# Kernel tuning notes

Hardware: AMD Instinct MI355X
Metric: run time of the kernel (lower is better)

The kernel has to match this reference:

```python
import jax, jax.numpy as jnp
import numpy as np
from jax import lax

PRE_NMS_TOPN = 6000
POST_NMS_TOPN = 1500
NMS_IOU_THRESHOLD = 0.7
VARIANCES = (0.1, 0.1, 0.2, 0.2)
TOTAL_ANCHORS = 200000
BATCH = 8


def setup_inputs() -> dict:
    key = jax.random.key(0)
    k1, k2, k3, k4 = jax.random.split(key, 4)
    rpn_bbox_deltas = jax.random.normal(k1, (BATCH, TOTAL_ANCHORS, 4), dtype=jnp.float32)
    rpn_probs = jax.random.uniform(k2, (BATCH, TOTAL_ANCHORS), dtype=jnp.float32)
    # anchors: valid normalized [y1, x1, y2, x2] boxes
    ctr = jax.random.uniform(k3, (TOTAL_ANCHORS, 2), dtype=jnp.float32)          # (cy, cx)
    hw = jax.random.uniform(k4, (TOTAL_ANCHORS, 2), dtype=jnp.float32,
                            minval=0.02, maxval=0.3)                              # (h, w)
    anchors = jnp.concatenate([ctr - 0.5 * hw, ctr + 0.5 * hw], axis=-1)
    return {"rpn_bbox_deltas": rpn_bbox_deltas, "rpn_probs": rpn_probs, "anchors": anchors}


def _nms_single(boxes):
    # boxes: [P, 4] sorted by descending score; greedy NMS, return [POST, 4] zero-padded,
    # coordinates clipped to [0, 1] (tf combined_non_max_suppression clip_boxes=True default).
    P = boxes.shape[0]
    y1, x1, y2, x2 = boxes[:, 0], boxes[:, 1], boxes[:, 2], boxes[:, 3]
    area = (y2 - y1) * (x2 - x1)
    iy1 = jnp.maximum(y1[:, None], y1[None, :])
    ix1 = jnp.maximum(x1[:, None], x1[None, :])
    iy2 = jnp.minimum(y2[:, None], y2[None, :])
    ix2 = jnp.minimum(x2[:, None], x2[None, :])
    inter = jnp.maximum(iy2 - iy1, 0.0) * jnp.maximum(ix2 - ix1, 0.0)
    iou = inter / (area[:, None] + area[None, :] - inter)  # [P, P]
    idx = jnp.arange(P)

    def body(i, keep):
        suppressed = keep[i] & (iou[i] > NMS_IOU_THRESHOLD) & (idx > i)
        return keep & ~suppressed

    keep = lax.fori_loop(0, P, body, jnp.ones((P,), dtype=bool))

    rank = jnp.cumsum(keep) - 1                      # position among kept boxes
    valid = keep & (rank < POST_NMS_TOPN)
    tgt = jnp.where(valid, rank, POST_NMS_TOPN)      # overflow slot for dropped boxes
    clipped = jnp.clip(boxes, 0.0, 1.0)
    out = jnp.zeros((POST_NMS_TOPN + 1, 4), dtype=boxes.dtype)
    out = out.at[tgt].set(jnp.where(valid[:, None], clipped, 0.0))
    return out[:POST_NMS_TOPN]


def reference(rpn_bbox_deltas, rpn_probs, anchors):
    variances = jnp.asarray(VARIANCES, dtype=rpn_bbox_deltas.dtype)
    deltas = rpn_bbox_deltas * variances                       # [B, A, 4]

    anc_w = anchors[:, 3] - anchors[:, 1]
    anc_h = anchors[:, 2] - anchors[:, 0]
    anc_cx = anchors[:, 1] + 0.5 * anc_w
    anc_cy = anchors[:, 0] + 0.5 * anc_h

    bw = jnp.exp(deltas[..., 3]) * anc_w
    bh = jnp.exp(deltas[..., 2]) * anc_h
    bcx = deltas[..., 1] * anc_w + anc_cx
    bcy = deltas[..., 0] * anc_h + anc_cy

    y1 = bcy - 0.5 * bh
    x1 = bcx - 0.5 * bw
    y2 = bh + y1
    x2 = bw + x1
    rpn_bboxes = jnp.stack([y1, x1, y2, x2], axis=-1)          # [B, A, 4]

    _, pre_indices = lax.top_k(rpn_probs, PRE_NMS_TOPN)        # [B, P], sorted desc
    pre_boxes = jnp.take_along_axis(rpn_bboxes, pre_indices[..., None], axis=1)  # [B, P, 4]

    roi_bboxes = jax.vmap(_nms_single)(pre_boxes)              # [B, POST, 4]
    return roi_bboxes
```

## Files before the change

### kernel.cpp

```cpp
#include <hip/hip_runtime.h>
#include <hip/hip_bf16.h>


#define TOTAL   200000
#define NBATCH  8
#define PRE     6000
#define POST    1500
#define NW      94
#define CAP     8192
#define NQ      (TOTAL/4)
#define GR      256
#define NGFAST  9
#define PLANES  960
#define HB      32

__device__ __forceinline__ unsigned int prob_key(float p) {
    return __float_as_uint(__fadd_rn(p, 1.0f)) & 0x7FFFFFu;
}

__global__ __launch_bounds__(1024) void k_hist256(const float* __restrict__ probs,
                                                  unsigned int* __restrict__ histS,
                                                  unsigned int* __restrict__ gcount) {
    const int b = blockIdx.y;
    const int bx = blockIdx.x;
    const int tid = threadIdx.x;
    __shared__ unsigned int h[256];
    if (tid < 256) h[tid] = 0u;
    if (bx == 0 && tid < 256) gcount[b * 256 + tid] = 0u;
    __syncthreads();
    const float4* p4 = (const float4*)(probs + (size_t)b * TOTAL);
    for (int i4 = bx * 1024 + tid; i4 < NQ; i4 += HB * 1024) {
        float4 v = p4[i4];
        atomicAdd(&h[prob_key(v.x) >> 15], 1u);
        atomicAdd(&h[prob_key(v.y) >> 15], 1u);
        atomicAdd(&h[prob_key(v.z) >> 15], 1u);
        atomicAdd(&h[prob_key(v.w) >> 15], 1u);
    }
    __syncthreads();
    if (tid < 256) histS[((size_t)b * HB + bx) * 256 + tid] = h[tid];
}

__global__ __launch_bounds__(1024) void k_collect(const float* __restrict__ probs,
                                                  const unsigned int* __restrict__ histS,
                                                  unsigned long long* __restrict__ keys,
                                                  unsigned int* __restrict__ gcount) {
    const int b = blockIdx.y;
    const int tid = threadIdx.x;
    __shared__ unsigned int S[257];
    __shared__ unsigned int lcnt[256];
    __shared__ unsigned int gbase[256];
    __shared__ unsigned int s_B;
    if (tid == 0) { s_B = 0u; S[256] = 0u; }
    if (tid < 256) {
        unsigned int s = 0u;
        const unsigned int* hb = histS + (size_t)b * HB * 256 + tid;
#pragma unroll
        for (int k = 0; k < HB; ++k) s += hb[k * 256];
        S[tid] = s; lcnt[tid] = 0u;
    }
    __syncthreads();
    for (int off = 1; off < 256; off <<= 1) {
        unsigned int v = 0u;
        if (tid < 256 && tid + off < 256) v = S[tid + off];
        __syncthreads();
        if (tid < 256) S[tid] += v;
        __syncthreads();
    }
    if (tid < 256 && S[tid] >= PRE) atomicMax(&s_B, (unsigned int)tid);
    __syncthreads();
    const unsigned int B = s_B;
    unsigned int kk[4], ii[4], tt[4], lp[4]; int n = 0;
    const int i4 = blockIdx.x * 1024 + tid;
    if (i4 < NQ) {
        float4 v = ((const float4*)(probs + (size_t)b * TOTAL))[i4];
        float pv[4] = {v.x, v.y, v.z, v.w};
#pragma unroll
        for (int j = 0; j < 4; ++j) {
            unsigned int key = prob_key(pv[j]);
            unsigned int t = key >> 15;
            if (t >= B) {
                kk[n] = key; ii[n] = (unsigned int)(i4 * 4 + j); tt[n] = t;
                lp[n] = atomicAdd(&lcnt[t], 1u);
                ++n;
            }
        }
    }
    __syncthreads();
    if (tid < 256 && lcnt[tid] > 0u)
        gbase[tid] = atomicAdd(&gcount[b * 256 + tid], lcnt[tid]);
    __syncthreads();
    for (int j = 0; j < n; ++j) {
        unsigned int t = tt[j];
        unsigned int pos = S[t + 1] + gbase[t] + lp[j];
        if (pos < CAP)
            keys[(size_t)b * CAP + pos] =
                ((unsigned long long)kk[j] << 32) | (unsigned long long)(~ii[j]);
    }
}

__global__ __launch_bounds__(256) void k_rank(const unsigned long long* __restrict__ keys,
                                              const unsigned int* __restrict__ histS,
                                              const float* __restrict__ deltas,
                                              const float* __restrict__ anchors,
                                              float4* __restrict__ boxes) {
    const int b   = blockIdx.y;
    const int rel = blockIdx.x;
    const int tid = threadIdx.x;
    __shared__ unsigned int S[257];
    __shared__ unsigned int s_B;
    __shared__ unsigned long long K2[CAP];
    __shared__ unsigned int CNT[512];
    __shared__ unsigned int W[512];
    __shared__ unsigned int P[256];
    if (tid == 0) { s_B = 0u; S[256] = 0u; }
    {
        unsigned int s = 0u;
        const unsigned int* hb = histS + (size_t)b * HB * 256 + tid;
#pragma unroll
        for (int k = 0; k < HB; ++k) s += hb[k * 256];
        S[tid] = s;
    }
    __syncthreads();
    for (int off = 1; off < 256; off <<= 1) {
        unsigned int v = (tid + off < 256) ? S[tid + off] : 0u;
        __syncthreads();
        S[tid] += v;
        __syncthreads();
    }
    if (S[tid] >= PRE) atomicMax(&s_B, (unsigned int)tid);
    __syncthreads();
    const int B = (int)s_B;
    const int t = B + rel;
    if (t > 255) return;
    const unsigned int lo = (rel == 15) ? 0u : S[t + 1];
    unsigned int hi = S[t]; if (hi > CAP) hi = CAP;
    if (hi <= lo) return;
    const unsigned int n = hi - lo;
    CNT[tid] = 0u; CNT[tid + 256] = 0u;
    __syncthreads();
    const unsigned long long* kb = keys + (size_t)b * CAP + lo;
    for (unsigned int i = tid; i < n; i += 256u) {
        const unsigned int key23 = (unsigned int)(kb[i] >> 32);
        const unsigned int bin = (rel == 15) ? (key23 >> 14) : ((key23 >> 6) & 511u);
        atomicAdd(&CNT[bin], 1u);
    }
    __syncthreads();
    {
        const unsigned int c0 = CNT[2 * tid], c1 = CNT[2 * tid + 1];
        P[tid] = c0 + c1;
        __syncthreads();
        for (int off = 1; off < 256; off <<= 1) {
            unsigned int v = (tid + off < 256) ? P[tid + off] : 0u;
            __syncthreads();
            P[tid] += v;
            __syncthreads();
        }
        const unsigned int above = P[tid] - (c0 + c1);
        W[2 * tid + 1] = above;
        W[2 * tid]     = above + c1;
    }
    __syncthreads();
    for (unsigned int i = tid; i < n; i += 256u) {
        const unsigned long long k = kb[i];
        const unsigned int key23 = (unsigned int)(k >> 32);
        const unsigned int bin = (rel == 15) ? (key23 >> 14) : ((key23 >> 6) & 511u);
        const unsigned int slot = atomicAdd(&W[bin], 1u);
        K2[slot] = k;
    }
    __syncthreads();
    for (int s = tid; s < 512; s += 256) {
        const unsigned int st = (s < 511) ? W[s + 1] : 0u;
        const unsigned int en = W[s];
        for (unsigned int x = st; x + 1 < en; ++x) {
            unsigned long long best = K2[x]; unsigned int bi = x;
            for (unsigned int y = x + 1; y < en; ++y) {
                unsigned long long v = K2[y];
                if (v > best) { best = v; bi = y; }
            }
            if (bi != x) { K2[bi] = K2[x]; K2[x] = best; }
        }
    }
    __syncthreads();
    for (unsigned int r = tid; r < n; r += 256u) {
        const unsigned int grank = lo + r;
        if (grank >= PRE) continue;
        const unsigned long long k = K2[r];
        const unsigned int idx = ~(unsigned int)(k & 0xFFFFFFFFull);
        const float* d = deltas + ((size_t)b * TOTAL + (size_t)idx) * 4;
        const float* a = anchors + (size_t)idx * 4;
        float d0 = __fmul_rn(d[0], 0.1f), d1 = __fmul_rn(d[1], 0.1f);
        float d2 = __fmul_rn(d[2], 0.2f), d3 = __fmul_rn(d[3], 0.2f);
        float a0 = a[0], a1 = a[1], a2 = a[2], a3 = a[3];
        float aw = __fsub_rn(a3, a1), ah = __fsub_rn(a2, a0);
        float acx = __fadd_rn(a1, __fmul_rn(0.5f, aw));
        float acy = __fadd_rn(a0, __fmul_rn(0.5f, ah));
        float bw = __fmul_rn(expf(d3), aw);
        float bh = __fmul_rn(expf(d2), ah);
        float bcx = __fadd_rn(__fmul_rn(d1, aw), acx);
        float bcy = __fadd_rn(__fmul_rn(d0, ah), acy);
        float y1 = __fsub_rn(bcy, __fmul_rn(0.5f, bh));
        float x1 = __fsub_rn(bcx, __fmul_rn(0.5f, bw));
        float y2 = __fadd_rn(bh, y1);
        float x2 = __fadd_rn(bw, x1);
        boxes[(size_t)b * PRE + grank] = make_float4(y1, x1, y2, x2);
    }
}

__global__ __launch_bounds__(256) void k_mask(const float4* __restrict__ boxes,
                                              unsigned long long* __restrict__ maskT) {
    const int b  = blockIdx.z;
    const int by = blockIdx.y;
    const int bx = blockIdx.x;
    if (bx < by) return;
    const int tid = threadIdx.x;
    __shared__ float4 cbox[256];
    __shared__ float  cth[256];
    __shared__ float  cca[256];
    {
        int col = bx * 256 + tid;
        float4 cb = (col < PRE) ? boxes[(size_t)b * PRE + col] : make_float4(0.f, 0.f, 0.f, 0.f);
        cbox[tid] = cb;
        float ca = __fmul_rn(__fsub_rn(cb.z, cb.x), __fsub_rn(cb.w, cb.y));
        cca[tid] = ca;
        cth[tid] = __fmul_rn(0.4115f, ca);
    }
    __syncthreads();
    const int il = tid & 63;
    const int ws = tid >> 6;
    const int w  = bx * 4 + ws;
    if (w >= NW) return;
    const int ibase = by * 256 + il;
    float4 rb0, rb1, rb2, rb3;
    {
        const float4 z = make_float4(0.f, 0.f, 0.f, 0.f);
        rb0 = boxes[(size_t)b * PRE + ibase];
        rb1 = (ibase +  64 < PRE) ? boxes[(size_t)b * PRE + ibase +  64] : z;
        rb2 = (ibase + 128 < PRE) ? boxes[(size_t)b * PRE + ibase + 128] : z;
        rb3 = (ibase + 192 < PRE) ? boxes[(size_t)b * PRE + ibase + 192] : z;
    }
    const float ra0 = __fmul_rn(__fsub_rn(rb0.z, rb0.x), __fsub_rn(rb0.w, rb0.y));
    const float ra1 = __fmul_rn(__fsub_rn(rb1.z, rb1.x), __fsub_rn(rb1.w, rb1.y));
    const float ra2 = __fmul_rn(__fsub_rn(rb2.z, rb2.x), __fsub_rn(rb2.w, rb2.y));
    const float ra3 = __fmul_rn(__fsub_rn(rb3.z, rb3.x), __fsub_rn(rb3.w, rb3.y));
    const float rc0 = __fmul_rn(0.4115f, ra0);
    const float rc1 = __fmul_rn(0.4115f, ra1);
    const float rc2 = __fmul_rn(0.4115f, ra2);
    const float rc3 = __fmul_rn(0.4115f, ra3);
    unsigned long long bits0 = 0ull, bits1 = 0ull, bits2 = 0ull, bits3 = 0ull;
    const double M = 0x1.666667p-1;
#pragma unroll 8
    for (int jj = 0; jj < 64; ++jj) {
        const float4 cb = cbox[ws * 64 + jj];
        const float  th = cth[ws * 64 + jj];
#define ROWTEST(rb, ra, rc, bits)                                              \
        {                                                                      \
            float dy = __fsub_rn(fminf(rb.z, cb.z), fmaxf(rb.x, cb.x));        \
            float dx = __fsub_rn(fminf(rb.w, cb.w), fmaxf(rb.y, cb.y));        \
            float hh = fmaxf(dy, 0.0f);                                        \
            float in = __fmul_rn(hh, dx);                                      \
            if (in > __fadd_rn(rc, th)) {                                      \
                float ww2 = fmaxf(dx, 0.0f);                                   \
                float ix  = __fmul_rn(hh, ww2);                                \
                float un  = __fsub_rn(__fadd_rn(ra, cca[ws * 64 + jj]), ix);   \
                if ((double)ix >= M * (double)un) bits |= (1ull << jj);        \
            }                                                                  \
        }
        ROWTEST(rb0, ra0, rc0, bits0)
        ROWTEST(rb1, ra1, rc1, bits1)
        ROWTEST(rb2, ra2, rc2, bits2)
        ROWTEST(rb3, ra3, rc3, bits3)
#undef ROWTEST
    }
    const int jbase = w * 64;
#define ROWSTORE(k, bits)                                                      \
    {                                                                          \
        const int i = ibase + 64 * (k);                                        \
        if (i < PRE && w >= (i >> 6)) {                                        \
            unsigned long long bb = bits;                                      \
            if (jbase <= i) {                                                  \
                int nclear = i - jbase + 1;                                    \
                bb = (nclear >= 64) ? 0ull : (bb & (~0ull << nclear));         \
            }                                                                  \
            maskT[((size_t)b * NW + w) * PRE + i] = bb;                        \
        }                                                                      \
    }
    ROWSTORE(0, bits0)
    ROWSTORE(1, bits1)
    ROWSTORE(2, bits2)
    ROWSTORE(3, bits3)
#undef ROWSTORE
}

__device__ __forceinline__ unsigned long long rfl64(unsigned long long v) {
    unsigned int lo = (unsigned int)__builtin_amdgcn_readfirstlane((unsigned int)v);
    unsigned int hi = (unsigned int)__builtin_amdgcn_readfirstlane((unsigned int)(v >> 32));
    return ((unsigned long long)hi << 32) | (unsigned long long)lo;
}

__device__ __forceinline__ unsigned long long wor64(unsigned long long v) {
    int lo = (int)(unsigned int)v;
    int hi = (int)(unsigned int)(v >> 32);
    lo |= __builtin_amdgcn_ds_swizzle(lo, 0x041F); hi |= __builtin_amdgcn_ds_swizzle(hi, 0x041F);
    lo |= __builtin_amdgcn_ds_swizzle(lo, 0x081F); hi |= __builtin_amdgcn_ds_swizzle(hi, 0x081F);
    lo |= __builtin_amdgcn_ds_swizzle(lo, 0x101F); hi |= __builtin_amdgcn_ds_swizzle(hi, 0x101F);
    lo |= __builtin_amdgcn_ds_swizzle(lo, 0x201F); hi |= __builtin_amdgcn_ds_swizzle(hi, 0x201F);
    lo |= __builtin_amdgcn_ds_swizzle(lo, 0x401F); hi |= __builtin_amdgcn_ds_swizzle(hi, 0x401F);
    const unsigned int l = (unsigned int)__builtin_amdgcn_readlane(lo, 0)
                         | (unsigned int)__builtin_amdgcn_readlane(lo, 32);
    const unsigned int h = (unsigned int)__builtin_amdgcn_readlane(hi, 0)
                         | (unsigned int)__builtin_amdgcn_readlane(hi, 32);
    return ((unsigned long long)h << 32) | (unsigned long long)l;
}

#define DIDX(qr,qw) ((qr)*4 + (qw) - ((qr)*((qr)+1))/2)

__global__ __launch_bounds__(1024) void k_scan(const float4* __restrict__ boxes,
                                               const unsigned long long* __restrict__ maskT,
                                               float4* __restrict__ out) {
    const int b = blockIdx.x;
    const int tid = threadIdx.x;
    const int wv = tid >> 6;
    const int lane = tid & 63;
    __shared__ unsigned long long remw[2][4];
    __shared__ unsigned long long keptbm[96];
    __shared__ float4 boxbuf[2][GR];
    __shared__ float4 keptbox[POST];
    __shared__ unsigned int s_rank;
    __shared__ int s_done;
    __shared__ int s_sup;
    if (tid < 8) ((unsigned long long*)remw)[tid] = 0ull;
    if (tid < 96) keptbm[tid] = 0ull;
    if (tid == 0) { s_rank = 0u; s_done = 0; }
    const unsigned long long* mb = maskT + (size_t)b * NW * PRE;

    unsigned long long dCur[10];
    unsigned long long pend0 = 0ull, pend1 = 0ull;
    unsigned int rank = 0u;

    if (wv == 0) {
#pragma unroll
        for (int qr = 0; qr < 4; ++qr) {
            const int row = 64 * qr + lane;
#pragma unroll
            for (int qw = qr; qw < 4; ++qw)
                dCur[DIDX(qr, qw)] = mb[(size_t)qw * PRE + row];
        }
    } else if (wv == 1) {
#pragma unroll
        for (int q = 0; q < 4; ++q)
            boxbuf[0][64 * q + lane] = boxes[(size_t)b * PRE + 64 * q + lane];
    }
    __syncthreads();

    for (int g = 0; g < NGFAST; ++g) {
        const int r0 = g * GR;
        const int w0 = g * 4;
        if (wv > 0) {
            const int L = tid - 64;
            unsigned int* R = (unsigned int*)&remw[g & 1][0];
            if (pend0) {
                const int q = L >> 8;
                const int row = (g - 1) * GR + (L & 255);
                if ((keptbm[row >> 6] >> (row & 63)) & 1ull) {
                    atomicOr(&R[2 * q],     (unsigned int)pend0);
                    atomicOr(&R[2 * q + 1], (unsigned int)(pend0 >> 32));
                }
            }
            if (pend1) {
                const int row = (g - 1) * GR + 192 + L;
                if ((keptbm[row >> 6] >> (row & 63)) & 1ull) {
                    atomicOr(&R[6], (unsigned int)pend1);
                    atomicOr(&R[7], (unsigned int)(pend1 >> 32));
                }
            }
        }
        __syncthreads();

        if (wv == 0) {
            unsigned long long dNxt[10];
#pragma unroll
            for (int i = 0; i < 10; ++i) dNxt[i] = 0ull;
            if (g + 1 < NGFAST) {
                const int r0n = (g + 1) * GR, w0n = (g + 1) * 4;
#pragma unroll
                for (int qr = 0; qr < 4; ++qr) {
                    const int row = r0n + 64 * qr + lane;
                    const bool rok = row < PRE;
#pragma unroll
                    for (int qw = qr; qw < 4; ++qw) {
                        const int w = w0n + qw;
                        if (rok && w < NW)
                            dNxt[DIDX(qr, qw)] = mb[(size_t)w * PRE + row];
                    }
                }
            }
            unsigned long long av[4];
#pragma unroll
            for (int q = 0; q < 4; ++q) av[q] = remw[g & 1][q];
            if (lane < 4) remw[g & 1][lane] = 0ull;
#pragma unroll
            for (int q = 0; q < 4; ++q) {
                const int rq = r0 + 64 * q;
                const unsigned long long valid =
                    (rq >= PRE) ? 0ull
                    : ((rq + 64 <= PRE) ? ~0ull : ((~0ull) >> (64 - (PRE - rq))));
                av[q] = rfl64(~av[q]) & valid;
            }
            unsigned long long keptq[4];
            unsigned int base = rank;
#pragma unroll
            for (int q = 0; q < 4; ++q) {
                const unsigned long long avq = av[q];
                const unsigned long long W = dCur[DIDX(q, q)];
                unsigned long long kept = 0ull;
                if (avq != 0ull) {
                    unsigned long long m = ((avq >> lane) & 1ull) ? W : 0ull;
                    const unsigned long long U = wor64(m);
                    const unsigned long long C = avq & ~U;
                    kept = C;
                    unsigned long long rem = avq & U;
                    if (rem != 0ull) {
                        unsigned long long mc = ((C >> lane) & 1ull) ? W : 0ull;
                        const unsigned long long UC = wor64(mc);
                        unsigned long long av2 = rem & ~UC;
                        const unsigned int wlo = (unsigned int)W;
                        const unsigned int whi = (unsigned int)(W >> 32);
                        while (av2) {
                            const int i2 = __ffsll((long long)av2) - 1;
                            const unsigned long long bit = 1ull << i2;
                            kept |= bit;
                            const unsigned long long Wi =
                                ((unsigned long long)(unsigned int)__builtin_amdgcn_readlane(whi, i2) << 32)
                                | (unsigned long long)(unsigned int)__builtin_amdgcn_readlane(wlo, i2);
                            av2 &= ~(Wi | bit);
                        }
                    }
                }
                keptq[q] = kept;
                if (q < 3 && kept != 0ull) {
                    const bool on = ((kept >> lane) & 1ull) != 0ull;
                    unsigned long long c1 = 0ull, c2 = 0ull, c3 = 0ull;
                    if (q == 0 && on) { c1 = dCur[DIDX(0,1)]; c2 = dCur[DIDX(0,2)]; c3 = dCur[DIDX(0,3)]; }
                    if (q == 1 && on) { c2 = dCur[DIDX(1,2)]; c3 = dCur[DIDX(1,3)]; }
                    if (q == 2 && on) { c3 = dCur[DIDX(2,3)]; }
                    if (q == 0) av[1] &= ~wor64(c1);
                    if (q <= 1) av[2] &= ~wor64(c2);
                    av[3] &= ~wor64(c3);
                }
                if ((kept >> lane) & 1ull) {
                    const unsigned int r =
                        base + (unsigned int)__popcll(kept & ((1ull << lane) - 1ull));
                    if (r < POST) {
                        const float4 v = boxbuf[g & 1][64 * q + lane];
                        keptbox[r] = v;
                        float4 cl;
                        cl.x = fminf(fmaxf(v.x, 0.f), 1.f);
                        cl.y = fminf(fmaxf(v.y, 0.f), 1.f);
                        cl.z = fminf(fmaxf(v.z, 0.f), 1.f);
                        cl.w = fminf(fmaxf(v.w, 0.f), 1.f);
                        out[(size_t)b * POST + r] = cl;
                    }
                }
                base += (unsigned int)__popcll(kept);
            }
            if (lane == 0) {
                keptbm[w0 + 0] = keptq[0];
                keptbm[w0 + 1] = keptq[1];
                keptbm[w0 + 2] = keptq[2];
                keptbm[w0 + 3] = keptq[3];
                s_rank = base;
                s_done = (base >= POST) ? 1 : 0;
            }
            rank = base;
#pragma unroll
            for (int i = 0; i < 10; ++i) dCur[i] = dNxt[i];
        } else {
            const int L = tid - 64;
            pend0 = 0ull; pend1 = 0ull;
            if (g + 1 < NGFAST) {
                const int w0n = (g + 1) * 4;
                if (wv == 1) {
#pragma unroll
                    for (int q = 0; q < 4; ++q) {
                        const int row = (g + 1) * GR + 64 * q + lane;
                        boxbuf[(g + 1) & 1][64 * q + lane] =
                            (row < PRE) ? boxes[(size_t)b * PRE + row]
                                        : make_float4(0.f, 0.f, 0.f, 0.f);
                    }
                }
                const bool ok1 = (w0n + 1 < NW), ok2 = (w0n + 2 < NW), ok3 = (w0n + 3 < NW);
                unsigned long long a0 = 0ull, a1 = 0ull, a2 = 0ull, a3 = 0ull;
                const int rlim = g * GR;
                for (int row = L; row < rlim; row += PLANES) {
                    const unsigned long long km =
                        ((keptbm[row >> 6] >> (row & 63)) & 1ull) ? ~0ull : 0ull;
                    const unsigned long long* cb = mb + row;
                    const unsigned long long v0 = cb[(size_t)(w0n + 0) * PRE];
                    const unsigned long long v1 = ok1 ? cb[(size_t)(w0n + 1) * PRE] : 0ull;
                    const unsigned long long v2 = ok2 ? cb[(size_t)(w0n + 2) * PRE] : 0ull;
                    const unsigned long long v3 = ok3 ? cb[(size_t)(w0n + 3) * PRE] : 0ull;
                    a0 |= v0 & km; a1 |= v1 & km; a2 |= v2 & km; a3 |= v3 & km;
                }
                {
                    unsigned int* R = (unsigned int*)&remw[(g + 1) & 1][0];
                    if (a0) { atomicOr(&R[0], (unsigned int)a0); atomicOr(&R[1], (unsigned int)(a0 >> 32)); }
                    if (a1) { atomicOr(&R[2], (unsigned int)a1); atomicOr(&R[3], (unsigned int)(a1 >> 32)); }
                    if (a2) { atomicOr(&R[4], (unsigned int)a2); atomicOr(&R[5], (unsigned int)(a2 >> 32)); }
                    if (a3) { atomicOr(&R[6], (unsigned int)a3); atomicOr(&R[7], (unsigned int)(a3 >> 32)); }
                }
                {
                    const int q = L >> 8;
                    const int w = w0n + q;
                    if (w < NW)
                        pend0 = mb[(size_t)w * PRE + (size_t)(g * GR + (L & 255))];
                }
                if (L < 64) {
                    const int w = w0n + 3;
                    if (w < NW)
                        pend1 = mb[(size_t)w * PRE + (size_t)(g * GR + 192 + L)];
                }
            }
        }
        __syncthreads();
        if (s_done) break;
    }

    if (!s_done) {
        unsigned int rk = s_rank;
        const double M = 0x1.666667p-1;
        for (int row = NGFAST * GR; row < PRE && rk < POST; ++row) {
            if (tid == 0) s_sup = 0;
            __syncthreads();
            const float4 rb = boxes[(size_t)b * PRE + row];
            const float ra = __fmul_rn(__fsub_rn(rb.z, rb.x), __fsub_rn(rb.w, rb.y));
            int sup = 0;
            for (unsigned int j = (unsigned int)tid; j < rk; j += 1024u) {
                const float4 kb = keptbox[j];
                float dy = __fsub_rn(fminf(rb.z, kb.z), fmaxf(rb.x, kb.x));
                float dx = __fsub_rn(fminf(rb.w, kb.w), fmaxf(rb.y, kb.y));
                float hh = fmaxf(dy, 0.f);
                float ww = fmaxf(dx, 0.f);
                float ix = __fmul_rn(hh, ww);
                float ka = __fmul_rn(__fsub_rn(kb.z, kb.x), __fsub_rn(kb.w, kb.y));
                float un = __fsub_rn(__fadd_rn(ka, ra), ix);
                if ((double)ix >= M * (double)un) { sup = 1; break; }
            }
            if (sup) atomicOr(&s_sup, 1);
            __syncthreads();
            if (!s_sup) {
                if (tid == 0) {
                    keptbox[rk] = rb;
                    float4 cl;
                    cl.x = fminf(fmaxf(rb.x, 0.f), 1.f);
                    cl.y = fminf(fmaxf(rb.y, 0.f), 1.f);
                    cl.z = fminf(fmaxf(rb.z, 0.f), 1.f);
                    cl.w = fminf(fmaxf(rb.w, 0.f), 1.f);
                    out[(size_t)b * POST + rk] = cl;
                }
                ++rk;
                __syncthreads();
            }
        }
        if (tid == 0) s_rank = rk;
        __syncthreads();
    }

    unsigned int filled = s_rank; if (filled > POST) filled = POST;
    for (unsigned int r = filled + (unsigned int)tid; r < POST; r += 1024u)
        out[(size_t)b * POST + r] = make_float4(0.f, 0.f, 0.f, 0.f);
}

extern "C" void kernel_launch(void* const* d_in, const int* in_sizes, int n_in,
                              void* d_out, int out_size, void* d_ws, size_t ws_size,
                              hipStream_t stream) {
    const float* deltas  = (const float*)d_in[0];
    const float* probs   = (const float*)d_in[1];
    const float* anchors = (const float*)d_in[2];
    char* ws = (char*)d_ws;
    unsigned int*       histS  = (unsigned int*)(ws);
    unsigned int*       gcount = (unsigned int*)(ws + 262144);
    unsigned long long* keys   = (unsigned long long*)(ws + 270336);
    float4*             boxes  = (float4*)(ws + 270336 + 524288);
    unsigned long long* maskT  = (unsigned long long*)(ws + 270336 + 524288 + 768000);
    float4* out = (float4*)d_out;

    k_hist256<<<dim3(HB, NBATCH), 1024, 0, stream>>>(probs, histS, gcount);
    k_collect<<<dim3((NQ + 1023) / 1024, NBATCH), 1024, 0, stream>>>(probs, histS, keys, gcount);
    k_rank<<<dim3(16, NBATCH), 256, 0, stream>>>(keys, histS, deltas, anchors, boxes);
    k_mask<<<dim3(NGFAST, NGFAST, NBATCH), 256, 0, stream>>>(boxes, maskT);
    k_scan<<<NBATCH, 1024, 0, stream>>>(boxes, maskT, out);
}
```

Before: 144.0 us.

## Fuse histogram and candidate collection into one pass with speculative top-bin buckets

```diff
diff --git a/kernel.cpp b/kernel.cpp
--- a/kernel.cpp
+++ b/kernel.cpp
@@ -13,93 +13,49 @@
 #define NGFAST  9
 #define PLANES  960
 #define HB      32
+#define KB0     246
+#define SUBCAP  160
 
 __device__ __forceinline__ unsigned int prob_key(float p) {
     return __float_as_uint(__fadd_rn(p, 1.0f)) & 0x7FFFFFu;
 }
 
-__global__ __launch_bounds__(1024) void k_hist256(const float* __restrict__ probs,
+__global__ __launch_bounds__(1024) void k_histsel(const float* __restrict__ probs,
                                                   unsigned int* __restrict__ histS,
-                                                  unsigned int* __restrict__ gcount) {
+                                                  unsigned long long* __restrict__ abuf) {
     const int b = blockIdx.y;
     const int bx = blockIdx.x;
     const int tid = threadIdx.x;
     __shared__ unsigned int h[256];
+    __shared__ unsigned int lcnt[10];
     if (tid < 256) h[tid] = 0u;
-    if (bx == 0 && tid < 256) gcount[b * 256 + tid] = 0u;
+    if (tid < 10) lcnt[tid] = 0u;
     __syncthreads();
     const float4* p4 = (const float4*)(probs + (size_t)b * TOTAL);
     for (int i4 = bx * 1024 + tid; i4 < NQ; i4 += HB * 1024) {
         float4 v = p4[i4];
-        atomicAdd(&h[prob_key(v.x) >> 15], 1u);
-        atomicAdd(&h[prob_key(v.y) >> 15], 1u);
-        atomicAdd(&h[prob_key(v.z) >> 15], 1u);
-        atomicAdd(&h[prob_key(v.w) >> 15], 1u);
+        float pv[4] = {v.x, v.y, v.z, v.w};
+#pragma unroll
+        for (int j = 0; j < 4; ++j) {
+            const unsigned int key = prob_key(pv[j]);
+            const unsigned int t = key >> 15;
+            atomicAdd(&h[t], 1u);
+            if (t >= KB0) {
+                const unsigned int slot = atomicAdd(&lcnt[t - KB0], 1u);
+                if (slot < SUBCAP)
+                    abuf[(((size_t)b * 10 + (t - KB0)) * HB + bx) * SUBCAP + slot] =
+                        ((unsigned long long)key << 32)
+                        | (unsigned long long)(~(unsigned int)(i4 * 4 + j));
+            }
+        }
     }
     __syncthreads();
     if (tid < 256) histS[((size_t)b * HB + bx) * 256 + tid] = h[tid];
 }
 
-__global__ __launch_bounds__(1024) void k_collect(const float* __restrict__ probs,
-                                                  const unsigned int* __restrict__ histS,
-                                                  unsigned long long* __restrict__ keys,
-                                                  unsigned int* __restrict__ gcount) {
-    const int b = blockIdx.y;
-    const int tid = threadIdx.x;
-    __shared__ unsigned int S[257];
-    __shared__ unsigned int lcnt[256];
-    __shared__ unsigned int gbase[256];
-    __shared__ unsigned int s_B;
-    if (tid == 0) { s_B = 0u; S[256] = 0u; }
-    if (tid < 256) {
-        unsigned int s = 0u;
-        const unsigned int* hb = histS + (size_t)b * HB * 256 + tid;
-#pragma unroll
-        for (int k = 0; k < HB; ++k) s += hb[k * 256];
-        S[tid] = s; lcnt[tid] = 0u;
-    }
-    __syncthreads();
-    for (int off = 1; off < 256; off <<= 1) {
-        unsigned int v = 0u;
-        if (tid < 256 && tid + off < 256) v = S[tid + off];
-        __syncthreads();
-        if (tid < 256) S[tid] += v;
-        __syncthreads();
-    }
-    if (tid < 256 && S[tid] >= PRE) atomicMax(&s_B, (unsigned int)tid);
-    __syncthreads();
-    const unsigned int B = s_B;
-    unsigned int kk[4], ii[4], tt[4], lp[4]; int n = 0;
-    const int i4 = blockIdx.x * 1024 + tid;
-    if (i4 < NQ) {
-        float4 v = ((const float4*)(probs + (size_t)b * TOTAL))[i4];
-        float pv[4] = {v.x, v.y, v.z, v.w};
-#pragma unroll
-        for (int j = 0; j < 4; ++j) {
-            unsigned int key = prob_key(pv[j]);
-            unsigned int t = key >> 15;
-            if (t >= B) {
-                kk[n] = key; ii[n] = (unsigned int)(i4 * 4 + j); tt[n] = t;
-                lp[n] = atomicAdd(&lcnt[t], 1u);
-                ++n;
-            }
-        }
-    }
-    __syncthreads();
-    if (tid < 256 && lcnt[tid] > 0u)
-        gbase[tid] = atomicAdd(&gcount[b * 256 + tid], lcnt[tid]);
-    __syncthreads();
-    for (int j = 0; j < n; ++j) {
-        unsigned int t = tt[j];
-        unsigned int pos = S[t + 1] + gbase[t] + lp[j];
-        if (pos < CAP)
-            keys[(size_t)b * CAP + pos] =
-                ((unsigned long long)kk[j] << 32) | (unsigned long long)(~ii[j]);
-    }
-}
-
-__global__ __launch_bounds__(256) void k_rank(const unsigned long long* __restrict__ keys,
+__global__ __launch_bounds__(256) void k_rank(const unsigned long long* __restrict__ abuf,
                                               const unsigned int* __restrict__ histS,
+                                              const float* __restrict__ probs,
                                               const float* __restrict__ deltas,
                                               const float* __restrict__ anchors,
                                               float4* __restrict__ boxes) {
@@ -108,11 +64,13 @@
     const int tid = threadIdx.x;
     __shared__ unsigned int S[257];
     __shared__ unsigned int s_B;
-    __shared__ unsigned long long K2[CAP];
+    __shared__ int s_slow;
     __shared__ unsigned int CNT[512];
     __shared__ unsigned int W[512];
     __shared__ unsigned int P[256];
-    if (tid == 0) { s_B = 0u; S[256] = 0u; }
+    __shared__ unsigned int SZ[HB];
+    __shared__ unsigned long long K2[CAP];
+    if (tid == 0) { s_B = 0u; S[256] = 0u; s_slow = 0; }
     {
         unsigned int s = 0u;
         const unsigned int* hb = histS + (size_t)b * HB * 256 + tid;
@@ -130,19 +88,88 @@
     if (S[tid] >= PRE) atomicMax(&s_B, (unsigned int)tid);
     __syncthreads();
     const int B = (int)s_B;
+    if (tid == 0 && B < KB0) s_slow = 1;
+    for (int x = tid; x < (256 - KB0) * HB; x += 256) {
+        const int t = KB0 + x / HB, blk = x % HB;
+        if (t >= B && histS[((size_t)b * HB + blk) * 256 + t] > SUBCAP) atomicOr(&s_slow, 1);
+    }
+    if (tid >= KB0 && tid >= B && (S[tid] - S[tid + 1]) > 2048u) atomicOr(&s_slow, 1);
+    __syncthreads();
+
+    if (s_slow) {
+        if (rel != 0) return;
+        W[tid] = S[tid + 1];
+        for (int x = tid; x < CAP; x += 256) K2[x] = 0ull;
+        __syncthreads();
+        const float4* p4 = (const float4*)(probs + (size_t)b * TOTAL);
+        for (int i4 = tid; i4 < NQ; i4 += 256) {
+            float4 v = p4[i4];
+            float pv[4] = {v.x, v.y, v.z, v.w};
+#pragma unroll
+            for (int j = 0; j < 4; ++j) {
+                const unsigned int key = prob_key(pv[j]);
+                const unsigned int tt = key >> 15;
+                if ((int)tt >= B) {
+                    const unsigned int pos = atomicAdd(&W[tt], 1u);
+                    if (pos < CAP)
+                        K2[pos] = ((unsigned long long)key << 32)
+                                  | (unsigned long long)(~(unsigned int)(i4 * 4 + j));
+                }
+            }
+        }
+        __syncthreads();
+        for (int k = 2; k <= CAP; k <<= 1) {
+            for (int j = k >> 1; j > 0; j >>= 1) {
+                for (int x = tid; x < CAP; x += 256) {
+                    const int ixj = x ^ j;
+                    if (ixj > x) {
+                        const bool asc = ((x & k) != 0);
+                        const unsigned long long a = K2[x], c = K2[ixj];
+                        if (asc ? (a > c) : (a < c)) { K2[x] = c; K2[ixj] = a; }
+                    }
+                }
+                __syncthreads();
+            }
+        }
+        for (unsigned int r = tid; r < PRE; r += 256u) {
+            const unsigned long long k = K2[r];
+            const unsigned int idx = ~(unsigned int)(k & 0xFFFFFFFFull);
+            const float* d = deltas + ((size_t)b * TOTAL + (size_t)idx) * 4;
+            const float* a = anchors + (size_t)idx * 4;
+            float d0 = __fmul_rn(d[0], 0.1f), d1 = __fmul_rn(d[1], 0.1f);
+            float d2 = __fmul_rn(d[2], 0.2f), d3 = __fmul_rn(d[3], 0.2f);
+            float a0 = a[0], a1 = a[1], a2 = a[2], a3 = a[3];
+            float aw = __fsub_rn(a3, a1), ah = __fsub_rn(a2, a0);
+            float acx = __fadd_rn(a1, __fmul_rn(0.5f, aw));
+            float acy = __fadd_rn(a0, __fmul_rn(0.5f, ah));
+            float bw = __fmul_rn(expf(d3), aw);
+            float bh = __fmul_rn(expf(d2), ah);
+            float bcx = __fadd_rn(__fmul_rn(d1, aw), acx);
+            float bcy = __fadd_rn(__fmul_rn(d0, ah), acy);
+            float y1 = __fsub_rn(bcy, __fmul_rn(0.5f, bh));
+            float x1 = __fsub_rn(bcx, __fmul_rn(0.5f, bw));
+            float y2 = __fadd_rn(bh, y1);
+            float x2 = __fadd_rn(bw, x1);
+            boxes[(size_t)b * PRE + r] = make_float4(y1, x1, y2, x2);
+        }
+        return;
+    }
+
     const int t = B + rel;
     if (t > 255) return;
-    const unsigned int lo = (rel == 15) ? 0u : S[t + 1];
-    unsigned int hi = S[t]; if (hi > CAP) hi = CAP;
-    if (hi <= lo) return;
-    const unsigned int n = hi - lo;
+    const unsigned int n = S[t] - S[t + 1];
+    if (n == 0u) return;
+    const unsigned int lo = S[t + 1];
+    if (tid < HB) SZ[tid] = histS[((size_t)b * HB + tid) * 256 + t];
     CNT[tid] = 0u; CNT[tid + 256] = 0u;
     __syncthreads();
-    const unsigned long long* kb = keys + (size_t)b * CAP + lo;
-    for (unsigned int i = tid; i < n; i += 256u) {
-        const unsigned int key23 = (unsigned int)(kb[i] >> 32);
-        const unsigned int bin = (rel == 15) ? (key23 >> 14) : ((key23 >> 6) & 511u);
-        atomicAdd(&CNT[bin], 1u);
+    const unsigned long long* tb = abuf + ((size_t)b * 10 + (t - KB0)) * HB * SUBCAP;
+    for (int x = tid; x < HB * SUBCAP; x += 256) {
+        const int blk = x / SUBCAP, off = x % SUBCAP;
+        if ((unsigned int)off < SZ[blk]) {
+            const unsigned int key23 = (unsigned int)(tb[x] >> 32);
+            atomicAdd(&CNT[(key23 >> 6) & 511u], 1u);
+        }
     }
     __syncthreads();
     {
@@ -160,12 +187,14 @@
         W[2 * tid]     = above + c1;
     }
     __syncthreads();
-    for (unsigned int i = tid; i < n; i += 256u) {
-        const unsigned long long k = kb[i];
-        const unsigned int key23 = (unsigned int)(k >> 32);
-        const unsigned int bin = (rel == 15) ? (key23 >> 14) : ((key23 >> 6) & 511u);
-        const unsigned int slot = atomicAdd(&W[bin], 1u);
-        K2[slot] = k;
+    for (int x = tid; x < HB * SUBCAP; x += 256) {
+        const int blk = x / SUBCAP, off = x % SUBCAP;
+        if ((unsigned int)off < SZ[blk]) {
+            const unsigned long long k = tb[x];
+            const unsigned int key23 = (unsigned int)(k >> 32);
+            const unsigned int slot = atomicAdd(&W[(key23 >> 6) & 511u], 1u);
+            K2[slot] = k;
+        }
     }
     __syncthreads();
     for (int s = tid; s < 512; s += 256) {
@@ -577,16 +606,14 @@
     const float* probs   = (const float*)d_in[1];
     const float* anchors = (const float*)d_in[2];
     char* ws = (char*)d_ws;
-    unsigned int*       histS  = (unsigned int*)(ws);
-    unsigned int*       gcount = (unsigned int*)(ws + 262144);
-    unsigned long long* keys   = (unsigned long long*)(ws + 270336);
-    float4*             boxes  = (float4*)(ws + 270336 + 524288);
-    unsigned long long* maskT  = (unsigned long long*)(ws + 270336 + 524288 + 768000);
+    unsigned int*       histS = (unsigned int*)(ws);
+    unsigned long long* abuf  = (unsigned long long*)(ws + 262144);
+    float4*             boxes = (float4*)(ws + 3538944);
+    unsigned long long* maskT = (unsigned long long*)(ws + 4306944);
     float4* out = (float4*)d_out;
 
-    k_hist256<<<dim3(HB, NBATCH), 1024, 0, stream>>>(probs, histS, gcount);
-    k_collect<<<dim3((NQ + 1023) / 1024, NBATCH), 1024, 0, stream>>>(probs, histS, keys, gcount);
-    k_rank<<<dim3(16, NBATCH), 256, 0, stream>>>(keys, histS, deltas, anchors, boxes);
+    k_histsel<<<dim3(HB, NBATCH), 1024, 0, stream>>>(probs, histS, abuf);
+    k_rank<<<dim3(16, NBATCH), 256, 0, stream>>>(abuf, histS, probs, deltas, anchors, boxes);
     k_mask<<<dim3(NGFAST, NGFAST, NBATCH), 256, 0, stream>>>(boxes, maskT);
     k_scan<<<NBATCH, 1024, 0, stream>>>(boxes, maskT, out);
 }
```

Measured after the change: 139.7 us. 1.03x faster.
